# Kernel tuning notes

Hardware: AMD Instinct MI355X
Metric: run time of the kernel (lower is better)

## Reference

```python
import jax, jax.numpy as jnp
import numpy as np

N, E, F_IN, D, H = 20000, 640000, 128, 16, 8  # nodes, edges, in_features, out_features, n_heads


def _linear_params(k, fan_in, fan_out):
    W = jax.random.normal(k, (fan_in, fan_out), jnp.float32) / np.sqrt(fan_in)
    b = jnp.zeros((fan_out,), jnp.float32)
    return W, b


def setup_inputs() -> dict:
    key = jax.random.key(0)
    ks = jax.random.split(key, 8)
    x = jax.random.normal(ks[0], (N, F_IN), jnp.float32)
    edge_index = jax.random.randint(ks[1], (2, E), 0, N, dtype=jnp.int64)
    Wq, bq = _linear_params(ks[2], F_IN, D * H)
    Wk, bk = _linear_params(ks[3], F_IN, D * H)
    Wv, bv = _linear_params(ks[4], F_IN, D * H)
    Wpsi, bpsi = _linear_params(ks[5], D, D)
    Wo, bo = _linear_params(ks[6], D * H * 2, F_IN)
    gamma = jnp.ones((F_IN,), jnp.float32)
    beta = jnp.zeros((F_IN,), jnp.float32)
    return {"x": x, "edge_index": edge_index, "Wq": Wq, "bq": bq, "Wk": Wk, "bk": bk,
            "Wv": Wv, "bv": bv, "Wpsi": Wpsi, "bpsi": bpsi, "Wo": Wo, "bo": bo,
            "gamma": gamma, "beta": beta}


def _segment_softmax(logits, seg, num_segments):
    # numerically-stable softmax of edge logits grouped by destination node (row)
    m = jax.ops.segment_max(logits, seg, num_segments=num_segments)  # [N,H]
    m = jnp.where(jnp.isfinite(m), m, 0.0)
    e = jnp.exp(logits - m[seg])  # [E,H]
    s = jax.ops.segment_sum(e, seg, num_segments=num_segments)  # [N,H]
    return e / (s[seg] + 1e-16)


def reference(x, edge_index, Wq, bq, Wk, bk, Wv, bv, Wpsi, bpsi, Wo, bo, gamma, beta):
    q = (x @ Wq + bq).reshape(N, H, D)
    k = (x @ Wk + bk).reshape(N, H, D)
    v = (x @ Wv + bv).reshape(N, H, D)
    row, col = edge_index[0], edge_index[1]

    logits = jnp.einsum('ehd,ehd->eh', q[row], k[col]) / np.sqrt(D)  # [E,H]
    alpha = _segment_softmax(logits, row, N)  # [E,H]

    v_j = v[col]  # [E,H,D]
    h_lp = jax.ops.segment_sum((alpha[..., None] * v_j).reshape(E, H * D), row, num_segments=N)
    v_bp = jnp.tanh(v_j @ Wpsi + bpsi)  # per-head linear on last dim, [E,H,D]
    h_bp = jax.ops.segment_sum((alpha[..., None] * v_bp).reshape(E, H * D), row, num_segments=N)

    h_out = jnp.concatenate([h_lp, h_bp], axis=1) @ Wo + bo  # [N,F_IN]
    y = x + jax.nn.relu(h_out)
    mu = jnp.mean(y, axis=-1, keepdims=True)
    var = jnp.mean(jnp.square(y - mu), axis=-1, keepdims=True)
    return (y - mu) * jax.lax.rsqrt(var + 1e-5) * gamma + beta
```

## Files before the change

kernel.cpp:

```cpp
#include <hip/hip_runtime.h>
#include <hip/hip_bf16.h>
#include <math.h>

#define NN 20000
#define EE 640000

typedef __attribute__((ext_vector_type(8))) short short8;
typedef __attribute__((ext_vector_type(4))) float f32x4;
typedef __hip_bfloat16 bf16;
typedef __hip_bfloat162 bf162;

__device__ inline ushort f2bf(float f) {
  bf16 h = __float2bfloat16(f);
  return *(ushort*)&h;
}
__device__ inline float2 ldbf2(const ushort* p) {
  return __bfloat1622float2(*(const bf162*)p);
}

__global__ __launch_bounds__(256) void qkv_mfma(
    const float* __restrict__ x,
    const float* __restrict__ Wq, const float* __restrict__ bq,
    const float* __restrict__ Wk, const float* __restrict__ bk,
    const float* __restrict__ Wv, const float* __restrict__ bv,
    float* __restrict__ qbuf, ushort* __restrict__ kvb) {
  __shared__ ushort As[128 * 136];
  __shared__ ushort Bts[128 * 136];
  int t = threadIdx.x;
  int n0 = blockIdx.x * 128;
  int mat = blockIdx.y;
  const float* W    = mat == 0 ? Wq : (mat == 1 ? Wk : Wv);
  const float* bias = mat == 0 ? bq : (mat == 1 ? bk : bv);

  {
    int r = t >> 1, half = (t & 1) * 64;
    int n = n0 + r;
    ushort* dst = &As[r * 136 + half];
    if (n < NN) {
      const float* src = x + (size_t)n * 128 + half;
#pragma unroll
      for (int j = 0; j < 8; ++j) {
        float4 f0 = *(const float4*)(src + 8 * j);
        float4 f1 = *(const float4*)(src + 8 * j + 4);
        ushort tmp[8] = {f2bf(f0.x), f2bf(f0.y), f2bf(f0.z), f2bf(f0.w),
                         f2bf(f1.x), f2bf(f1.y), f2bf(f1.z), f2bf(f1.w)};
        *(uint4*)(dst + 8 * j) = *(uint4*)tmp;
      }
    } else {
#pragma unroll
      for (int j = 0; j < 8; ++j) *(uint4*)(dst + 8 * j) = make_uint4(0, 0, 0, 0);
    }
  }
  {
    int k = t >> 1, nh = (t & 1) * 64;
    const float* src = W + (size_t)k * 128 + nh;
#pragma unroll
    for (int i = 0; i < 16; ++i) {
      float4 f = *(const float4*)(src + 4 * i);
      Bts[(nh + 4 * i + 0) * 136 + k] = f2bf(f.x);
      Bts[(nh + 4 * i + 1) * 136 + k] = f2bf(f.y);
      Bts[(nh + 4 * i + 2) * 136 + k] = f2bf(f.z);
      Bts[(nh + 4 * i + 3) * 136 + k] = f2bf(f.w);
    }
  }
  __syncthreads();

  int w = t >> 6, lane = t & 63;
  int m = lane & 15, q = lane >> 4;
  int r0 = w * 32;
  f32x4 acc0[8], acc1[8];
#pragma unroll
  for (int c = 0; c < 8; ++c) {
    acc0[c] = (f32x4){0.f, 0.f, 0.f, 0.f};
    acc1[c] = (f32x4){0.f, 0.f, 0.f, 0.f};
  }
#pragma unroll
  for (int kb = 0; kb < 4; ++kb) {
    int kof = kb * 32 + 8 * q;
    short8 a0 = *(const short8*)&As[(r0 + m) * 136 + kof];
    short8 a1 = *(const short8*)&As[(r0 + 16 + m) * 136 + kof];
#pragma unroll
    for (int c = 0; c < 8; ++c) {
      short8 b = *(const short8*)&Bts[(c * 16 + m) * 136 + kof];
      acc0[c] = __builtin_amdgcn_mfma_f32_16x16x32_bf16(a0, b, acc0[c], 0, 0, 0);
      acc1[c] = __builtin_amdgcn_mfma_f32_16x16x32_bf16(a1, b, acc1[c], 0, 0, 0);
    }
  }
  int koff = (mat == 2) ? 128 : 0;
#pragma unroll
  for (int c = 0; c < 8; ++c) {
    int col = c * 16 + m;
    float bb = bias[col];
#pragma unroll
    for (int reg = 0; reg < 4; ++reg) {
      int row0 = n0 + r0 + 4 * q + reg;
      int row1 = row0 + 16;
      float v0 = acc0[c][reg] + bb;
      float v1 = acc1[c][reg] + bb;
      if (mat == 0) {
        if (row0 < NN) qbuf[(size_t)row0 * 128 + col] = v0;
        if (row1 < NN) qbuf[(size_t)row1 * 128 + col] = v1;
      } else {
        if (row0 < NN) kvb[(size_t)row0 * 384 + koff + col] = f2bf(v0);
        if (row1 < NN) kvb[(size_t)row1 * 384 + koff + col] = f2bf(v1);
      }
    }
  }
}

__global__ __launch_bounds__(256) void vb_kernel(
    ushort* __restrict__ kvb,
    const float* __restrict__ Wpsi, const float* __restrict__ bpsi) {
  __shared__ float Ws[256];
  __shared__ float bs[16];
  int t = threadIdx.x;
  Ws[t] = Wpsi[t];
  if (t < 16) bs[t] = bpsi[t];
  __syncthreads();
  int idx = blockIdx.x * 256 + t;
  int n = idx >> 3, h = idx & 7;
  ushort* base = kvb + (size_t)n * 384;
  const ushort* vp = base + 128 + h * 16;
  float v[16];
#pragma unroll
  for (int j = 0; j < 8; ++j) {
    float2 f = ldbf2(vp + 2 * j);
    v[2 * j] = f.x; v[2 * j + 1] = f.y;
  }
  float o[16];
#pragma unroll
  for (int d = 0; d < 16; ++d) o[d] = bs[d];
#pragma unroll
  for (int dp = 0; dp < 16; ++dp) {
    float vv = v[dp];
#pragma unroll
    for (int d = 0; d < 16; ++d) o[d] = fmaf(vv, Ws[dp * 16 + d], o[d]);
  }
  ushort* dst = base + 256 + h * 16;
#pragma unroll
  for (int j = 0; j < 8; ++j) {
    uint u = (uint)f2bf(tanhf(o[2 * j])) | ((uint)f2bf(tanhf(o[2 * j + 1])) << 16);
    *(uint*)(dst + 2 * j) = u;
  }
}

__global__ __launch_bounds__(256) void scatter_pad(const int* __restrict__ ei,
                                                   int* __restrict__ cursor,
                                                   int* __restrict__ scol) {
  int e = blockIdx.x * 256 + threadIdx.x;
  if (e < EE) {
    int r = ei[e];
    int c = ei[EE + e];
    int pos = atomicAdd(&cursor[r], 1);
    if (pos < 128) scol[r * 128 + pos] = c;
  }
}

__global__ __launch_bounds__(256) void aggregate_kernel(
    const float* __restrict__ qbuf, const ushort* __restrict__ kvb,
    const int* __restrict__ cursor, const int* __restrict__ scol,
    float* __restrict__ hbuf) {
  int wid = threadIdx.x >> 6, lane = threadIdx.x & 63;
  int node = blockIdx.x * 4 + wid;
  int h = lane >> 3, dg = (lane & 7) * 2;
  int off = h * 16 + dg;
  const float SC = 0.25f * 1.44269504f;
  float2 q2 = *(const float2*)(qbuf + (size_t)node * 128 + off);
  q2.x *= SC; q2.y *= SC;
  int cnt = cursor[node];
  cnt = cnt > 128 ? 128 : cnt;
  int base = node * 128;
  float s = 0.f, aV0 = 0.f, aV1 = 0.f, aB0 = 0.f, aB1 = 0.f;

  auto proc = [&](int j) {
    const ushort* B = kvb + (size_t)j * 384 + off;
    float2 kk = ldbf2(B);
    float2 vv = ldbf2(B + 128);
    float2 tb = ldbf2(B + 256);
    float d = fmaf(q2.x, kk.x, q2.y * kk.y);
    d += __shfl_xor(d, 1);
    d += __shfl_xor(d, 2);
    d += __shfl_xor(d, 4);
    float wgt = exp2f(d);
    s += wgt;
    aV0 = fmaf(wgt, vv.x, aV0); aV1 = fmaf(wgt, vv.y, aV1);
    aB0 = fmaf(wgt, tb.x, aB0); aB1 = fmaf(wgt, tb.y, aB1);
  };
  int i = 0;
  for (; i + 4 <= cnt; i += 4) {
    int4 js = *(const int4*)&scol[base + i];
    proc(js.x); proc(js.y); proc(js.z); proc(js.w);
  }
  for (; i < cnt; ++i) proc(scol[base + i]);

  float inv = s > 0.f ? 1.f / s : 0.f;
  float* hp = hbuf + (size_t)node * 256 + off;
  *(float2*)(hp)       = make_float2(aV0 * inv, aV1 * inv);
  *(float2*)(hp + 128) = make_float2(aB0 * inv, aB1 * inv);
}

__global__ __launch_bounds__(256) void output_mfma(
    const float* __restrict__ hbuf, const float* __restrict__ x,
    const float* __restrict__ Wo, const float* __restrict__ bo,
    const float* __restrict__ gamma, const float* __restrict__ beta,
    float* __restrict__ out) {
  __shared__ ushort As[128 * 136];
  __shared__ ushort Bts[128 * 136];
  __shared__ float bos[128], gs[128], bts[128];
  int t = threadIdx.x;
  int n0 = blockIdx.x * 128;
  if (t < 128) { bos[t] = bo[t]; gs[t] = gamma[t]; bts[t] = beta[t]; }
  int w = t >> 6, lane = t & 63;
  int m = lane & 15, q = lane >> 4;
  int r0 = w * 32;
  f32x4 acc0[8], acc1[8];
#pragma unroll
  for (int c = 0; c < 8; ++c) {
    acc0[c] = (f32x4){0.f, 0.f, 0.f, 0.f};
    acc1[c] = (f32x4){0.f, 0.f, 0.f, 0.f};
  }
  for (int kc = 0; kc < 2; ++kc) {
    if (kc) __syncthreads();
    {
      int r = t >> 1, half = (t & 1) * 64;
      int n = n0 + r;
      ushort* dst = &As[r * 136 + half];
      if (n < NN) {
        const float* src = hbuf + (size_t)n * 256 + kc * 128 + half;
#pragma unroll
        for (int j = 0; j < 8; ++j) {
          float4 f0 = *(const float4*)(src + 8 * j);
          float4 f1 = *(const float4*)(src + 8 * j + 4);
          ushort tmp[8] = {f2bf(f0.x), f2bf(f0.y), f2bf(f0.z), f2bf(f0.w),
                           f2bf(f1.x), f2bf(f1.y), f2bf(f1.z), f2bf(f1.w)};
          *(uint4*)(dst + 8 * j) = *(uint4*)tmp;
        }
      } else {
#pragma unroll
        for (int j = 0; j < 8; ++j) *(uint4*)(dst + 8 * j) = make_uint4(0, 0, 0, 0);
      }
    }
    {
      int k = t >> 1, nh = (t & 1) * 64;
      const float* src = Wo + (size_t)(kc * 128 + k) * 128 + nh;
#pragma unroll
      for (int i = 0; i < 16; ++i) {
        float4 f = *(const float4*)(src + 4 * i);
        Bts[(nh + 4 * i + 0) * 136 + k] = f2bf(f.x);
        Bts[(nh + 4 * i + 1) * 136 + k] = f2bf(f.y);
        Bts[(nh + 4 * i + 2) * 136 + k] = f2bf(f.z);
        Bts[(nh + 4 * i + 3) * 136 + k] = f2bf(f.w);
      }
    }
    __syncthreads();
#pragma unroll
    for (int kb = 0; kb < 4; ++kb) {
      int kof = kb * 32 + 8 * q;
      short8 a0 = *(const short8*)&As[(r0 + m) * 136 + kof];
      short8 a1 = *(const short8*)&As[(r0 + 16 + m) * 136 + kof];
#pragma unroll
      for (int c = 0; c < 8; ++c) {
        short8 b = *(const short8*)&Bts[(c * 16 + m) * 136 + kof];
        acc0[c] = __builtin_amdgcn_mfma_f32_16x16x32_bf16(a0, b, acc0[c], 0, 0, 0);
        acc1[c] = __builtin_amdgcn_mfma_f32_16x16x32_bf16(a1, b, acc1[c], 0, 0, 0);
      }
    }
  }
#pragma unroll
  for (int half = 0; half < 2; ++half) {
#pragma unroll
    for (int reg = 0; reg < 4; ++reg) {
      int row = n0 + r0 + half * 16 + 4 * q + reg;
      bool valid = row < NN;
      float vals[8];
      float sum = 0.f;
#pragma unroll
      for (int c = 0; c < 8; ++c) {
        int col = c * 16 + m;
        float a = (half ? acc1[c][reg] : acc0[c][reg]) + bos[col];
        a = fmaxf(a, 0.f);
        float xv = valid ? x[(size_t)row * 128 + col] : 0.f;
        float v = a + xv;
        vals[c] = v;
        sum += v;
      }
      sum += __shfl_xor(sum, 1); sum += __shfl_xor(sum, 2);
      sum += __shfl_xor(sum, 4); sum += __shfl_xor(sum, 8);
      float mean = sum * (1.f / 128.f);
      float ssq = 0.f;
#pragma unroll
      for (int c = 0; c < 8; ++c) {
        float d = vals[c] - mean;
        ssq = fmaf(d, d, ssq);
      }
      ssq += __shfl_xor(ssq, 1); ssq += __shfl_xor(ssq, 2);
      ssq += __shfl_xor(ssq, 4); ssq += __shfl_xor(ssq, 8);
      float rstd = rsqrtf(ssq * (1.f / 128.f) + 1e-5f);
      if (valid) {
#pragma unroll
        for (int c = 0; c < 8; ++c) {
          int col = c * 16 + m;
          out[(size_t)row * 128 + col] = (vals[c] - mean) * rstd * gs[col] + bts[col];
        }
      }
    }
  }
}

extern "C" void kernel_launch(void* const* d_in, const int* in_sizes, int n_in,
                              void* d_out, int out_size, void* d_ws, size_t ws_size,
                              hipStream_t stream) {
  const float* x     = (const float*)d_in[0];
  const int*   ei    = (const int*)d_in[1];
  const float* Wq    = (const float*)d_in[2];
  const float* bq    = (const float*)d_in[3];
  const float* Wk    = (const float*)d_in[4];
  const float* bk    = (const float*)d_in[5];
  const float* Wv    = (const float*)d_in[6];
  const float* bv    = (const float*)d_in[7];
  const float* Wpsi  = (const float*)d_in[8];
  const float* bpsi  = (const float*)d_in[9];
  const float* Wo    = (const float*)d_in[10];
  const float* bo    = (const float*)d_in[11];
  const float* gamma = (const float*)d_in[12];
  const float* beta  = (const float*)d_in[13];
  float* out = (float*)d_out;

  char* ws = (char*)d_ws;
  float*  qbuf   = (float*) (ws);
  ushort* kvb    = (ushort*)(ws + 10240000);
  float*  hbuf   = (float*) (ws + 25600000);
  int*    cursor = (int*)   (ws + 46080000);
  int*    scol   = (int*)   (ws + 46160000);

  hipMemsetAsync(cursor, 0, 80000, stream);

  qkv_mfma<<<dim3(157, 3), 256, 0, stream>>>(x, Wq, bq, Wk, bk, Wv, bv, qbuf, kvb);
  vb_kernel<<<625, 256, 0, stream>>>(kvb, Wpsi, bpsi);
  scatter_pad<<<2500, 256, 0, stream>>>(ei, cursor, scol);
  aggregate_kernel<<<5000, 256, 0, stream>>>(qbuf, kvb, cursor, scol, hbuf);
  output_mfma<<<157, 256, 0, stream>>>(hbuf, x, Wo, bo, gamma, beta, out);
}
```

Before: 227.9 us.

## Interleave K/V/Vb per lane in kvb and batch 8 gathers in aggregate

Reorders the per-node bf16 K, V and tanh(V·Wpsi) buffer so each lane's k, v and vb pairs sit contiguously in 12 bytes, letting aggregate fetch all three with a single 96-bit load per neighbor. The QKV epilogue and vb kernel write and read the new interleaved layout. The aggregate loop is also unrolled to issue 8 neighbor loads before processing them, raising memory-level parallelism. Costs are strided, less coalesced writes in the producer kernels and higher register pressure in aggregate.

```diff
diff --git a/kernel.cpp b/kernel.cpp
--- a/kernel.cpp
+++ b/kernel.cpp
@@ -17,6 +17,10 @@
 __device__ inline float2 ldbf2(const ushort* p) {
   return __bfloat1622float2(*(const bf162*)p);
 }
+__device__ inline float2 bf2u(uint u) {
+  return __bfloat1622float2(*(const bf162*)&u);
+}
+
 
 __global__ __launch_bounds__(256) void qkv_mfma(
     const float* __restrict__ x,
@@ -86,11 +90,12 @@
       acc1[c] = __builtin_amdgcn_mfma_f32_16x16x32_bf16(a1, b, acc1[c], 0, 0, 0);
     }
   }
-  int koff = (mat == 2) ? 128 : 0;
+  int koff2 = (mat == 2) ? 2 : 0;
 #pragma unroll
   for (int c = 0; c < 8; ++c) {
     int col = c * 16 + m;
     float bb = bias[col];
+    size_t pos = (size_t)(col >> 1) * 6 + (col & 1) + koff2;
 #pragma unroll
     for (int reg = 0; reg < 4; ++reg) {
       int row0 = n0 + r0 + 4 * q + reg;
@@ -101,8 +106,8 @@
         if (row0 < NN) qbuf[(size_t)row0 * 128 + col] = v0;
         if (row1 < NN) qbuf[(size_t)row1 * 128 + col] = v1;
       } else {
-        if (row0 < NN) kvb[(size_t)row0 * 384 + koff + col] = f2bf(v0);
-        if (row1 < NN) kvb[(size_t)row1 * 384 + koff + col] = f2bf(v1);
+        if (row0 < NN) kvb[(size_t)row0 * 384 + pos] = f2bf(v0);
+        if (row1 < NN) kvb[(size_t)row1 * 384 + pos] = f2bf(v1);
       }
     }
   }
@@ -119,13 +124,12 @@
   __syncthreads();
   int idx = blockIdx.x * 256 + t;
   int n = idx >> 3, h = idx & 7;
-  ushort* base = kvb + (size_t)n * 384;
-  const ushort* vp = base + 128 + h * 16;
+  ushort* base = kvb + (size_t)n * 384 + (size_t)h * 48;
   float v[16];
 #pragma unroll
-  for (int j = 0; j < 8; ++j) {
-    float2 f = ldbf2(vp + 2 * j);
-    v[2 * j] = f.x; v[2 * j + 1] = f.y;
+  for (int dp = 0; dp < 8; ++dp) {
+    float2 f = ldbf2(base + dp * 6 + 2);
+    v[2 * dp] = f.x; v[2 * dp + 1] = f.y;
   }
   float o[16];
 #pragma unroll
@@ -136,11 +140,10 @@
 #pragma unroll
     for (int d = 0; d < 16; ++d) o[d] = fmaf(vv, Ws[dp * 16 + d], o[d]);
   }
-  ushort* dst = base + 256 + h * 16;
-#pragma unroll
-  for (int j = 0; j < 8; ++j) {
-    uint u = (uint)f2bf(tanhf(o[2 * j])) | ((uint)f2bf(tanhf(o[2 * j + 1])) << 16);
-    *(uint*)(dst + 2 * j) = u;
+#pragma unroll
+  for (int dp = 0; dp < 8; ++dp) {
+    uint u = (uint)f2bf(tanhf(o[2 * dp])) | ((uint)f2bf(tanhf(o[2 * dp + 1])) << 16);
+    *(uint*)(base + dp * 6 + 4) = u;
   }
 }
 
@@ -170,13 +173,17 @@
   int cnt = cursor[node];
   cnt = cnt > 128 ? 128 : cnt;
   int base = node * 128;
+  const char* kvbase = (const char*)kvb + lane * 12;
   float s = 0.f, aV0 = 0.f, aV1 = 0.f, aB0 = 0.f, aB1 = 0.f;
 
-  auto proc = [&](int j) {
-    const ushort* B = kvb + (size_t)j * 384 + off;
-    float2 kk = ldbf2(B);
-    float2 vv = ldbf2(B + 128);
-    float2 tb = ldbf2(B + 256);
+  struct U3 { uint x, y, z; };
+  auto ldu = [&](int j) -> U3 {
+    return *(const U3*)(kvbase + (size_t)j * 768);
+  };
+  auto proc = [&](U3 u) {
+    float2 kk = bf2u(u.x);
+    float2 vv = bf2u(u.y);
+    float2 tb = bf2u(u.z);
     float d = fmaf(q2.x, kk.x, q2.y * kk.y);
     d += __shfl_xor(d, 1);
     d += __shfl_xor(d, 2);
@@ -186,12 +193,23 @@
     aV0 = fmaf(wgt, vv.x, aV0); aV1 = fmaf(wgt, vv.y, aV1);
     aB0 = fmaf(wgt, tb.x, aB0); aB1 = fmaf(wgt, tb.y, aB1);
   };
+
   int i = 0;
-  for (; i + 4 <= cnt; i += 4) {
-    int4 js = *(const int4*)&scol[base + i];
-    proc(js.x); proc(js.y); proc(js.z); proc(js.w);
-  }
-  for (; i < cnt; ++i) proc(scol[base + i]);
+  for (; i + 8 <= cnt; i += 8) {
+    int4 ja = *(const int4*)&scol[base + i];
+    int4 jb = *(const int4*)&scol[base + i + 4];
+    U3 u0 = ldu(ja.x), u1 = ldu(ja.y), u2 = ldu(ja.z), u3 = ldu(ja.w);
+    U3 u4 = ldu(jb.x), u5 = ldu(jb.y), u6 = ldu(jb.z), u7 = ldu(jb.w);
+    proc(u0); proc(u1); proc(u2); proc(u3);
+    proc(u4); proc(u5); proc(u6); proc(u7);
+  }
+  if (i + 4 <= cnt) {
+    int4 ja = *(const int4*)&scol[base + i];
+    U3 u0 = ldu(ja.x), u1 = ldu(ja.y), u2 = ldu(ja.z), u3 = ldu(ja.w);
+    proc(u0); proc(u1); proc(u2); proc(u3);
+    i += 4;
+  }
+  for (; i < cnt; ++i) proc(ldu(scol[base + i]));
 
   float inv = s > 0.f ? 1.f / s : 0.f;
   float* hp = hbuf + (size_t)node * 256 + off;
```

Result: slower. 235.4 us (+3.3%).

## Interleave K/V/tanh layout and process eight edges per wave in aggregation

Applied to the files above, without the earlier changes.

The K, V and tanh(V) bf16 rows are stored in a permuted dimension layout so each lane can read a head's 16 values as 16-byte vector loads. The aggregation kernel now assigns each lane a (head, edge-slot) pair and handles eight edges at once, with a full 16-wide dot product per lane instead of a shuffle reduction per edge. Edge batches are double-buffered so loads overlap compute. Partial sums are combined with cross-lane shuffles at the end, which adds register pressure and masked padding work when node degree is low.

```diff
diff --git a/kernel.cpp b/kernel.cpp
--- a/kernel.cpp
+++ b/kernel.cpp
@@ -17,6 +17,9 @@
 __device__ inline float2 ldbf2(const ushort* p) {
   return __bfloat1622float2(*(const bf162*)p);
 }
+__device__ inline float bflo(uint u) { return __uint_as_float(u << 16); }
+__device__ inline float bfhi(uint u) { return __uint_as_float(u & 0xffff0000u); }
+
 
 __global__ __launch_bounds__(256) void qkv_mfma(
     const float* __restrict__ x,
@@ -86,11 +89,11 @@
       acc1[c] = __builtin_amdgcn_mfma_f32_16x16x32_bf16(a1, b, acc1[c], 0, 0, 0);
     }
   }
-  int koff = (mat == 2) ? 128 : 0;
 #pragma unroll
   for (int c = 0; c < 8; ++c) {
     int col = c * 16 + m;
     float bb = bias[col];
+    size_t pos = (size_t)((m >> 3) * 64 + c * 8 + (m & 7)) + (mat == 2 ? 128 : 0);
 #pragma unroll
     for (int reg = 0; reg < 4; ++reg) {
       int row0 = n0 + r0 + 4 * q + reg;
@@ -101,8 +104,8 @@
         if (row0 < NN) qbuf[(size_t)row0 * 128 + col] = v0;
         if (row1 < NN) qbuf[(size_t)row1 * 128 + col] = v1;
       } else {
-        if (row0 < NN) kvb[(size_t)row0 * 384 + koff + col] = f2bf(v0);
-        if (row1 < NN) kvb[(size_t)row1 * 384 + koff + col] = f2bf(v1);
+        if (row0 < NN) kvb[(size_t)row0 * 384 + pos] = f2bf(v0);
+        if (row1 < NN) kvb[(size_t)row1 * 384 + pos] = f2bf(v1);
       }
     }
   }
@@ -120,12 +123,15 @@
   int idx = blockIdx.x * 256 + t;
   int n = idx >> 3, h = idx & 7;
   ushort* base = kvb + (size_t)n * 384;
-  const ushort* vp = base + 128 + h * 16;
+  const ushort* vp0 = base + 128 + h * 8;
+  const ushort* vp1 = base + 192 + h * 8;
   float v[16];
 #pragma unroll
-  for (int j = 0; j < 8; ++j) {
-    float2 f = ldbf2(vp + 2 * j);
-    v[2 * j] = f.x; v[2 * j + 1] = f.y;
+  for (int j = 0; j < 4; ++j) {
+    float2 f0 = ldbf2(vp0 + 2 * j);
+    float2 f1 = ldbf2(vp1 + 2 * j);
+    v[2 * j] = f0.x; v[2 * j + 1] = f0.y;
+    v[8 + 2 * j] = f1.x; v[8 + 2 * j + 1] = f1.y;
   }
   float o[16];
 #pragma unroll
@@ -136,11 +142,14 @@
 #pragma unroll
     for (int d = 0; d < 16; ++d) o[d] = fmaf(vv, Ws[dp * 16 + d], o[d]);
   }
-  ushort* dst = base + 256 + h * 16;
-#pragma unroll
-  for (int j = 0; j < 8; ++j) {
-    uint u = (uint)f2bf(tanhf(o[2 * j])) | ((uint)f2bf(tanhf(o[2 * j + 1])) << 16);
-    *(uint*)(dst + 2 * j) = u;
+  ushort* bp0 = base + 256 + h * 8;
+  ushort* bp1 = base + 320 + h * 8;
+#pragma unroll
+  for (int j = 0; j < 4; ++j) {
+    uint u0 = (uint)f2bf(tanhf(o[2 * j])) | ((uint)f2bf(tanhf(o[2 * j + 1])) << 16);
+    uint u1 = (uint)f2bf(tanhf(o[8 + 2 * j])) | ((uint)f2bf(tanhf(o[8 + 2 * j + 1])) << 16);
+    *(uint*)(bp0 + 2 * j) = u0;
+    *(uint*)(bp1 + 2 * j) = u1;
   }
 }
 
@@ -162,41 +171,114 @@
     float* __restrict__ hbuf) {
   int wid = threadIdx.x >> 6, lane = threadIdx.x & 63;
   int node = blockIdx.x * 4 + wid;
-  int h = lane >> 3, dg = (lane & 7) * 2;
-  int off = h * 16 + dg;
+  int h = lane & 7, g = lane >> 3;
   const float SC = 0.25f * 1.44269504f;
-  float2 q2 = *(const float2*)(qbuf + (size_t)node * 128 + off);
-  q2.x *= SC; q2.y *= SC;
+
+  float qf[16];
+  {
+    const float* qp = qbuf + (size_t)node * 128 + h * 16;
+#pragma unroll
+    for (int j = 0; j < 4; ++j) {
+      float4 f = *(const float4*)(qp + 4 * j);
+      qf[4 * j + 0] = f.x * SC; qf[4 * j + 1] = f.y * SC;
+      qf[4 * j + 2] = f.z * SC; qf[4 * j + 3] = f.w * SC;
+    }
+  }
   int cnt = cursor[node];
   cnt = cnt > 128 ? 128 : cnt;
-  int base = node * 128;
-  float s = 0.f, aV0 = 0.f, aV1 = 0.f, aB0 = 0.f, aB1 = 0.f;
-
-  auto proc = [&](int j) {
-    const ushort* B = kvb + (size_t)j * 384 + off;
-    float2 kk = ldbf2(B);
-    float2 vv = ldbf2(B + 128);
-    float2 tb = ldbf2(B + 256);
-    float d = fmaf(q2.x, kk.x, q2.y * kk.y);
-    d += __shfl_xor(d, 1);
-    d += __shfl_xor(d, 2);
-    d += __shfl_xor(d, 4);
-    float wgt = exp2f(d);
+  int sbase = node * 128;
+  const char* kvbase = (const char*)kvb;
+  int hb = h * 16;
+
+  float s = 0.f;
+  float aV[16], aB[16];
+#pragma unroll
+  for (int j = 0; j < 16; ++j) { aV[j] = 0.f; aB[j] = 0.f; }
+
+  auto ldbatch = [&](int i, uint4 (&L)[6], bool& val) {
+    int idx = i + g;
+    bool v = idx < cnt;
+    int idx2 = v ? idx : (cnt - 1);
+    int e = scol[sbase + idx2];
+    const char* rb = kvbase + (size_t)e * 768 + hb;
+#pragma unroll
+    for (int j = 0; j < 6; ++j) L[j] = *(const uint4*)(rb + 128 * j);
+    val = v;
+  };
+
+  auto proc = [&](uint4 (&L)[6], bool val) {
+    uint k8[8];
+    *(uint4*)&k8[0] = L[0]; *(uint4*)&k8[4] = L[1];
+    float d0 = 0.f, d1 = 0.f;
+#pragma unroll
+    for (int j = 0; j < 8; ++j) {
+      uint u = k8[j];
+      d0 = fmaf(bflo(u), qf[2 * j], d0);
+      d1 = fmaf(bfhi(u), qf[2 * j + 1], d1);
+    }
+    float wgt = exp2f(d0 + d1);
+    wgt = val ? wgt : 0.f;
     s += wgt;
-    aV0 = fmaf(wgt, vv.x, aV0); aV1 = fmaf(wgt, vv.y, aV1);
-    aB0 = fmaf(wgt, tb.x, aB0); aB1 = fmaf(wgt, tb.y, aB1);
+    uint v8[8];
+    *(uint4*)&v8[0] = L[2]; *(uint4*)&v8[4] = L[3];
+#pragma unroll
+    for (int j = 0; j < 8; ++j) {
+      uint u = v8[j];
+      aV[2 * j]     = fmaf(bflo(u), wgt, aV[2 * j]);
+      aV[2 * j + 1] = fmaf(bfhi(u), wgt, aV[2 * j + 1]);
+    }
+    uint b8[8];
+    *(uint4*)&b8[0] = L[4]; *(uint4*)&b8[4] = L[5];
+#pragma unroll
+    for (int j = 0; j < 8; ++j) {
+      uint u = b8[j];
+      aB[2 * j]     = fmaf(bflo(u), wgt, aB[2 * j]);
+      aB[2 * j + 1] = fmaf(bfhi(u), wgt, aB[2 * j + 1]);
+    }
   };
-  int i = 0;
-  for (; i + 4 <= cnt; i += 4) {
-    int4 js = *(const int4*)&scol[base + i];
-    proc(js.x); proc(js.y); proc(js.z); proc(js.w);
-  }
-  for (; i < cnt; ++i) proc(scol[base + i]);
-
+
+  if (cnt > 0) {
+    int nbatch = (cnt + 7) >> 3;
+    uint4 A[6], B[6];
+    bool av = false, bv = false;
+    ldbatch(0, A, av);
+    int b = 0;
+    for (; b + 2 < nbatch; b += 2) {
+      ldbatch((b + 1) * 8, B, bv);
+      proc(A, av);
+      ldbatch((b + 2) * 8, A, av);
+      proc(B, bv);
+    }
+    if (b + 1 < nbatch) {
+      ldbatch((b + 1) * 8, B, bv);
+      proc(A, av);
+      proc(B, bv);
+    } else {
+      proc(A, av);
+    }
+  }
+
+#pragma unroll
+  for (int mask = 8; mask <= 32; mask <<= 1) {
+    s += __shfl_xor(s, mask);
+#pragma unroll
+    for (int j = 0; j < 16; ++j) {
+      aV[j] += __shfl_xor(aV[j], mask);
+      aB[j] += __shfl_xor(aB[j], mask);
+    }
+  }
   float inv = s > 0.f ? 1.f / s : 0.f;
-  float* hp = hbuf + (size_t)node * 256 + off;
-  *(float2*)(hp)       = make_float2(aV0 * inv, aV1 * inv);
-  *(float2*)(hp + 128) = make_float2(aB0 * inv, aB1 * inv);
+  float r0, r1, r2, r3;
+  if (g == 0)      { r0 = aV[0];  r1 = aV[1];  r2 = aV[2];  r3 = aV[3];  }
+  else if (g == 1) { r0 = aV[4];  r1 = aV[5];  r2 = aV[6];  r3 = aV[7];  }
+  else if (g == 2) { r0 = aV[8];  r1 = aV[9];  r2 = aV[10]; r3 = aV[11]; }
+  else if (g == 3) { r0 = aV[12]; r1 = aV[13]; r2 = aV[14]; r3 = aV[15]; }
+  else if (g == 4) { r0 = aB[0];  r1 = aB[1];  r2 = aB[2];  r3 = aB[3];  }
+  else if (g == 5) { r0 = aB[4];  r1 = aB[5];  r2 = aB[6];  r3 = aB[7];  }
+  else if (g == 6) { r0 = aB[8];  r1 = aB[9];  r2 = aB[10]; r3 = aB[11]; }
+  else             { r0 = aB[12]; r1 = aB[13]; r2 = aB[14]; r3 = aB[15]; }
+  float* hp = hbuf + (size_t)node * 256 + (g < 4 ? 0 : 128) + h * 16 + (g & 3) * 4;
+  *(float4*)hp = make_float4(r0 * inv, r1 * inv, r2 * inv, r3 * inv);
 }
 
 __global__ __launch_bounds__(256) void output_mfma(
```

After: 231.8 us. About the same (+1.7%).
